# Optimization experiments

Measured on AMD Instinct MI355X. Metric: run time of the kernel, lower is better.

## Reference

```python
import jax, jax.numpy as jnp
import numpy as np

K = 16  # FLAGS.num_neighbors
N = 2562  # ellipsoid vertices
B = 4     # FLAGS.batch_size
M = 16384 # points per cloud
D = 3     # coordinate dim


def _mean_neighborhood(coord, pc, k):
    # coord: [N, D] query vertices; pc: [B, D, M] point cloud (channels-first)
    x2 = jnp.sum(coord * coord, axis=1)[None, :, None]          # [1, N, 1]
    y2 = jnp.sum(pc * pc, axis=1)[:, None, :]                   # [B, 1, M]
    xy = jnp.einsum('nd,bdm->bnm', coord, pc)                   # [B, N, M]
    d2 = x2 + y2 - 2.0 * xy                                     # [B, N, M]
    _, idx = jax.lax.top_k(-d2, k)                               # [B, N, K] indices into M
    Y = jnp.transpose(pc, (0, 2, 1))                             # [B, M, D]
    bv = jnp.arange(pc.shape[0])[:, None, None]                  # [B, 1, 1]
    knnY = Y[bv, idx]                                            # [B, N, K, D]
    knnY_mean = jnp.mean(knnY, axis=2)                           # [B, N, D]
    return knnY_mean[0]                                          # [N, D] (matches knnY_mean[0])


def setup_inputs() -> dict:
    key = jax.random.key(0)
    ks = jax.random.split(key, 5)
    inputs = jax.random.normal(ks[0], (N, D), dtype=jnp.float32)
    pcs = [jax.random.normal(ks[i + 1], (B, D, M), dtype=jnp.float32) for i in range(4)]
    return {"inputs": inputs, "pc0": pcs[0], "pc1": pcs[1], "pc2": pcs[2], "pc3": pcs[3]}


def reference(inputs, pc0, pc1, pc2, pc3):
    s0 = _mean_neighborhood(inputs, pc0, K)
    s1 = _mean_neighborhood(inputs, pc1, K)
    s2 = _mean_neighborhood(inputs, pc2, K)
    s3 = _mean_neighborhood(inputs, pc3, K)
    return jnp.concatenate([inputs, s0, s1, s2, s3], axis=1)  # [N, 5*D]
```

## Files before the change

kernel.cpp:

```cpp
#include <hip/hip_runtime.h>
#include <stdint.h>
#include <math.h>

#define NQ    2562
#define MPTS  16384
#define QPB   8
#define NBQ   321
#define NT    (MPTS / 256)
#define CAP   320

__global__ __launch_bounds__(256)
void passthrough_kernel(const float* __restrict__ inp, float* __restrict__ out) {
    int gid = blockIdx.x * 256 + threadIdx.x;
    if (gid < NQ * 3) {
        int n = gid / 3, c = gid - n * 3;
        out[n * 15 + c] = inp[gid];
    }
}

__device__ __forceinline__ float sqsum3(float y0, float y1, float y2) {
    return __fadd_rn(__fadd_rn(__fmul_rn(y0, y0), __fmul_rn(y1, y1)),
                     __fmul_rn(y2, y2));
}
__device__ __forceinline__ float keyf(float xs, float a2, float b2, float c2,
                                      float y0, float y1, float y2, float ysq) {
    float u = fmaf(c2, y2, fmaf(b2, y1, __fmul_rn(a2, y0)));
    return __fsub_rn(__fadd_rn(xs, ysq), u);
}
__device__ __forceinline__ unsigned long long packkey(float k, int m) {
    uint32_t kb = __float_as_uint(k);
    kb ^= (uint32_t)((int32_t)kb >> 31) | 0x80000000u;
    return ((unsigned long long)kb << 32) | (unsigned)m;
}
__device__ __forceinline__ float unmapkey(unsigned long long pk) {
    uint32_t kb = (uint32_t)(pk >> 32);
    return __uint_as_float((kb & 0x80000000u) ? (kb ^ 0x80000000u) : ~kb);
}
__device__ __forceinline__ int prefix_lt(unsigned long long m) {
    return __builtin_amdgcn_mbcnt_hi((unsigned)(m >> 32),
           __builtin_amdgcn_mbcnt_lo((unsigned)m, 0u));
}

__device__ __forceinline__ unsigned long long sort64(unsigned long long v, int lane) {
#pragma unroll
    for (int k = 2; k <= 64; k <<= 1) {
#pragma unroll
        for (int j = k >> 1; j > 0; j >>= 1) {
            unsigned long long p = __shfl_xor(v, j);
            bool up = ((lane & k) == 0) == ((lane & j) == 0);
            bool sw = up ? (p < v) : (v < p);
            v = sw ? p : v;
        }
    }
    return v;
}

__device__ __forceinline__ float rebuild_q(unsigned long long* t16p,
                                           unsigned* S, int& cnt, int lane,
                                           const float* __restrict__ P,
                                           float xs, float a2, float b2, float c2,
                                           bool fin) {
    int c = cnt;
    int full = c >> 6, rem = c & 63;
    int rounds = full + ((fin && rem) ? 1 : 0);
    unsigned long long v = ~0ULL;
    for (int rd = 0; rd < rounds; ++rd) {
        int i = (rd << 6) + lane;
        unsigned idx = (i < c) ? S[i] : 0u;
        float y0 = P[idx], y1 = P[MPTS + idx], y2 = P[2 * MPTS + idx];
        float key = keyf(xs, a2, b2, c2, y0, y1, y2, sqsum3(y0, y1, y2));
        unsigned long long pk = (i < c) ? packkey(key, (int)idx) : ~0ULL;
        pk = sort64(pk, lane);
        unsigned long long bsw = __shfl(pk, (31 - lane) & 63);
        v = (lane < 16) ? t16p[lane & 15] : (lane < 32) ? bsw : ~0ULL;
#pragma unroll
        for (int j = 16; j > 0; j >>= 1) {
            unsigned long long p2 = __shfl_xor(v, j);
            bool keepmin = (lane & j) == 0;
            bool less = p2 < v;
            v = (keepmin == less) ? p2 : v;
        }
        if (lane < 16) t16p[lane] = v;
    }
    if (!fin) {
        if (lane < rem) S[lane] = S[(full << 6) + lane];
        cnt = rem;
    } else {
        cnt = 0;
    }
    return unmapkey(__shfl(v, 15));
}

__global__ __launch_bounds__(256)
void knn_kernel(const float* __restrict__ inp,
                const float* __restrict__ pc0, const float* __restrict__ pc1,
                const float* __restrict__ pc2, const float* __restrict__ pc3,
                float* __restrict__ out) {
    const int b    = blockIdx.x;
    const int wid  = threadIdx.x >> 6;
    const int lane = threadIdx.x & 63;

    const int pc = b / NBQ;
    const int nb = b - pc * NBQ;
    const float* __restrict__ P = (pc == 0) ? pc0 : (pc == 1) ? pc1
                                : (pc == 2) ? pc2 : pc3;

    __shared__ unsigned           stk_sh[4][2][CAP];
    __shared__ unsigned long long t16_sh[4][2][16];

    if (lane < 32) t16_sh[wid][lane >> 4][lane & 15] = ~0ULL;

    float A2[2], B2[2], C2[2], XS[2];
#pragma unroll
    for (int r = 0; r < 2; ++r) {
        int n = QPB * nb + 2 * wid + r;
        n = (n < NQ) ? n : (NQ - 1);
        float x0 = inp[n * 3 + 0];
        float x1 = inp[n * 3 + 1];
        float x2 = inp[n * 3 + 2];
        A2[r] = 2.0f * x0;
        B2[r] = 2.0f * x1;
        C2[r] = 2.0f * x2;
        XS[r] = sqsum3(x0, x1, x2);
    }
    float tau[2];
    int   cnt[2] = {0, 0};

    const float* __restrict__ Pl = P + (lane << 2);

    auto push_tile = [&](int r, int mofs, float k0, float k1, float k2, float k3) {
        unsigned long long b0 = __ballot(k0 <= tau[r]);
        unsigned long long b1 = __ballot(k1 <= tau[r]);
        unsigned long long b2 = __ballot(k2 <= tau[r]);
        unsigned long long b3 = __ballot(k3 <= tau[r]);
        int pre = prefix_lt(b0) + prefix_lt(b1) + prefix_lt(b2) + prefix_lt(b3);
        int tot = __popcll(b0) + __popcll(b1) + __popcll(b2) + __popcll(b3);
        int pos = cnt[r] + pre;
        unsigned* S = stk_sh[wid][r];
        if (k0 <= tau[r]) S[pos++] = (unsigned)(mofs + 0);
        if (k1 <= tau[r]) S[pos++] = (unsigned)(mofs + 1);
        if (k2 <= tau[r]) S[pos++] = (unsigned)(mofs + 2);
        if (k3 <= tau[r]) S[pos++] = (unsigned)(mofs + 3);
        cnt[r] += tot;
        if (cnt[r] >= 64)
            tau[r] = rebuild_q(t16_sh[wid][r], S, cnt[r], lane,
                               P, XS[r], A2[r], B2[r], C2[r], false);
    };

    {
        float4 ax = *(const float4*)(Pl);
        float4 ay = *(const float4*)(Pl + MPTS);
        float4 az = *(const float4*)(Pl + 2 * MPTS);
        float q0 = sqsum3(ax.x, ay.x, az.x);
        float q1 = sqsum3(ax.y, ay.y, az.y);
        float q2 = sqsum3(ax.z, ay.z, az.z);
        float q3 = sqsum3(ax.w, ay.w, az.w);
#pragma unroll
        for (int r = 0; r < 2; ++r) {
            float k0 = keyf(XS[r], A2[r], B2[r], C2[r], ax.x, ay.x, az.x, q0);
            float k1 = keyf(XS[r], A2[r], B2[r], C2[r], ax.y, ay.y, az.y, q1);
            float k2 = keyf(XS[r], A2[r], B2[r], C2[r], ax.z, ay.z, az.z, q2);
            float k3 = keyf(XS[r], A2[r], B2[r], C2[r], ax.w, ay.w, az.w, q3);
            float km = fminf(fminf(k0, k1), fminf(k2, k3));
            float g = km;
            g = fminf(g, __shfl_xor(g, 1));
            g = fminf(g, __shfl_xor(g, 2));
            float m = g;
            m = fmaxf(m, __shfl_xor(m, 4));
            m = fmaxf(m, __shfl_xor(m, 8));
            m = fmaxf(m, __shfl_xor(m, 16));
            m = fmaxf(m, __shfl_xor(m, 32));
            tau[r] = m;
            push_tile(r, lane << 2, k0, k1, k2, k3);
        }
    }

    float4 cx = *(const float4*)(Pl + 256);
    float4 cy = *(const float4*)(Pl + MPTS + 256);
    float4 cz = *(const float4*)(Pl + 2 * MPTS + 256);

    for (int t = 1; t < NT; ++t) {
        const int tn = (t + 1 < NT) ? t + 1 : t;
        float4 nx = *(const float4*)(Pl + (tn << 8));
        float4 ny = *(const float4*)(Pl + MPTS + (tn << 8));
        float4 nz = *(const float4*)(Pl + 2 * MPTS + (tn << 8));

        const int mofs = (t << 8) + (lane << 2);
        float q0 = sqsum3(cx.x, cy.x, cz.x);
        float q1 = sqsum3(cx.y, cy.y, cz.y);
        float q2 = sqsum3(cx.z, cy.z, cz.z);
        float q3 = sqsum3(cx.w, cy.w, cz.w);
#pragma unroll
        for (int r = 0; r < 2; ++r) {
            float k0 = keyf(XS[r], A2[r], B2[r], C2[r], cx.x, cy.x, cz.x, q0);
            float k1 = keyf(XS[r], A2[r], B2[r], C2[r], cx.y, cy.y, cz.y, q1);
            float k2 = keyf(XS[r], A2[r], B2[r], C2[r], cx.z, cy.z, cz.z, q2);
            float k3 = keyf(XS[r], A2[r], B2[r], C2[r], cx.w, cy.w, cz.w, q3);
            float km = fminf(fminf(k0, k1), fminf(k2, k3));
            if (__ballot(km <= tau[r]))
                push_tile(r, mofs, k0, k1, k2, k3);
        }
        cx = nx; cy = ny; cz = nz;
    }

#pragma unroll
    for (int r = 0; r < 2; ++r) {
        if (cnt[r] > 0)
            rebuild_q(t16_sh[wid][r], stk_sh[wid][r], cnt[r], lane,
                      P, XS[r], A2[r], B2[r], C2[r], true);
    }

    {
        const int h   = lane >> 5;
        const int l32 = lane & 31;
        if (l32 < 16) {
            unsigned long long v = t16_sh[wid][h][l32];
            int idx = (int)(unsigned)v;
            float gx = P[idx];
            float gy = P[MPTS + idx];
            float gz = P[2 * MPTS + idx];
#pragma unroll
            for (int off = 8; off > 0; off >>= 1) {
                gx += __shfl_down(gx, off, 16);
                gy += __shfl_down(gy, off, 16);
                gz += __shfl_down(gz, off, 16);
            }
            if (l32 == 0) {
                int n = QPB * nb + 2 * wid + h;
                n = (n < NQ) ? n : (NQ - 1);
                float* o = out + n * 15 + 3 + 3 * pc;
                o[0] = gx * 0.0625f;
                o[1] = gy * 0.0625f;
                o[2] = gz * 0.0625f;
            }
        }
    }
}

extern "C" void kernel_launch(void* const* d_in, const int* in_sizes, int n_in,
                              void* d_out, int out_size, void* d_ws, size_t ws_size,
                              hipStream_t stream) {
    const float* inp = (const float*)d_in[0];
    const float* pc0 = (const float*)d_in[1];
    const float* pc1 = (const float*)d_in[2];
    const float* pc2 = (const float*)d_in[3];
    const float* pc3 = (const float*)d_in[4];
    float* out = (float*)d_out;

    hipLaunchKernelGGL(passthrough_kernel, dim3((NQ * 3 + 255) / 256), dim3(256),
                       0, stream, inp, out);

    hipLaunchKernelGGL(knn_kernel, dim3(4 * NBQ), dim3(256), 0, stream,
                       inp, pc0, pc1, pc2, pc3, out);
}
```

Before: 107.8 us.

## Process 512-point tiles per iteration and halve block size to 128 threads

Each warp now processes 8 candidate points per lane per iteration (two float4 groups 256 apart), so loop overhead and the ballot early-out check are amortized over twice as many points. Blocks shrink to 2 wavefronts (4 queries), doubling the block count, and the candidate stack capacity grows to hold up to 8 pushes per tile. The initial tau is now taken from the minimum over 8 points per lane, which makes it looser and can let more candidates through to rebuilds. Register pressure also rises from the extra prefetched float4s.

```diff
diff --git a/kernel.cpp b/kernel.cpp
--- a/kernel.cpp
+++ b/kernel.cpp
@@ -4,10 +4,10 @@
 
 #define NQ    2562
 #define MPTS  16384
-#define QPB   8
-#define NBQ   321
-#define NT    (MPTS / 256)
-#define CAP   320
+#define QPB   4
+#define NBQ   641
+#define NT    (MPTS / 512)
+#define CAP   576
 
 __global__ __launch_bounds__(256)
 void passthrough_kernel(const float* __restrict__ inp, float* __restrict__ out) {
@@ -91,7 +91,7 @@
     return unmapkey(__shfl(v, 15));
 }
 
-__global__ __launch_bounds__(256)
+__global__ __launch_bounds__(128)
 void knn_kernel(const float* __restrict__ inp,
                 const float* __restrict__ pc0, const float* __restrict__ pc1,
                 const float* __restrict__ pc2, const float* __restrict__ pc3,
@@ -105,8 +105,8 @@
     const float* __restrict__ P = (pc == 0) ? pc0 : (pc == 1) ? pc1
                                 : (pc == 2) ? pc2 : pc3;
 
-    __shared__ unsigned           stk_sh[4][2][CAP];
-    __shared__ unsigned long long t16_sh[4][2][16];
+    __shared__ unsigned           stk_sh[2][2][CAP];
+    __shared__ unsigned long long t16_sh[2][2][16];
 
     if (lane < 32) t16_sh[wid][lane >> 4][lane & 15] = ~0ULL;
 
@@ -128,79 +128,82 @@
 
     const float* __restrict__ Pl = P + (lane << 2);
 
-    auto push_tile = [&](int r, int mofs, float k0, float k1, float k2, float k3) {
-        unsigned long long b0 = __ballot(k0 <= tau[r]);
-        unsigned long long b1 = __ballot(k1 <= tau[r]);
-        unsigned long long b2 = __ballot(k2 <= tau[r]);
-        unsigned long long b3 = __ballot(k3 <= tau[r]);
-        int pre = prefix_lt(b0) + prefix_lt(b1) + prefix_lt(b2) + prefix_lt(b3);
-        int tot = __popcll(b0) + __popcll(b1) + __popcll(b2) + __popcll(b3);
+    auto push8 = [&](int r, int base0, const float* k) {
+        unsigned long long bm[8];
+        int pre = 0, tot = 0;
+#pragma unroll
+        for (int i = 0; i < 8; ++i) {
+            bm[i] = __ballot(k[i] <= tau[r]);
+            pre += prefix_lt(bm[i]);
+            tot += __popcll(bm[i]);
+        }
         int pos = cnt[r] + pre;
         unsigned* S = stk_sh[wid][r];
-        if (k0 <= tau[r]) S[pos++] = (unsigned)(mofs + 0);
-        if (k1 <= tau[r]) S[pos++] = (unsigned)(mofs + 1);
-        if (k2 <= tau[r]) S[pos++] = (unsigned)(mofs + 2);
-        if (k3 <= tau[r]) S[pos++] = (unsigned)(mofs + 3);
+#pragma unroll
+        for (int i = 0; i < 8; ++i)
+            if (k[i] <= tau[r]) S[pos++] = (unsigned)(base0 + (i < 4 ? i : i + 252));
         cnt[r] += tot;
         if (cnt[r] >= 64)
             tau[r] = rebuild_q(t16_sh[wid][r], S, cnt[r], lane,
                                P, XS[r], A2[r], B2[r], C2[r], false);
     };
 
-    {
-        float4 ax = *(const float4*)(Pl);
-        float4 ay = *(const float4*)(Pl + MPTS);
-        float4 az = *(const float4*)(Pl + 2 * MPTS);
-        float q0 = sqsum3(ax.x, ay.x, az.x);
-        float q1 = sqsum3(ax.y, ay.y, az.y);
-        float q2 = sqsum3(ax.z, ay.z, az.z);
-        float q3 = sqsum3(ax.w, ay.w, az.w);
+    float4 cx0, cx1, cy0, cy1, cz0, cz1;
+    cx0 = *(const float4*)(Pl);             cx1 = *(const float4*)(Pl + 256);
+    cy0 = *(const float4*)(Pl + MPTS);      cy1 = *(const float4*)(Pl + MPTS + 256);
+    cz0 = *(const float4*)(Pl + 2*MPTS);    cz1 = *(const float4*)(Pl + 2*MPTS + 256);
+
+    for (int t = 0; t < NT; ++t) {
+        const int tn = (t + 1 < NT) ? t + 1 : t;
+        const int po = tn << 9;
+        float4 nx0 = *(const float4*)(Pl + po);
+        float4 nx1 = *(const float4*)(Pl + po + 256);
+        float4 ny0 = *(const float4*)(Pl + MPTS + po);
+        float4 ny1 = *(const float4*)(Pl + MPTS + po + 256);
+        float4 nz0 = *(const float4*)(Pl + 2*MPTS + po);
+        float4 nz1 = *(const float4*)(Pl + 2*MPTS + po + 256);
+
+        const int base0 = (t << 9) + (lane << 2);
+        float q[8];
+        q[0] = sqsum3(cx0.x, cy0.x, cz0.x);
+        q[1] = sqsum3(cx0.y, cy0.y, cz0.y);
+        q[2] = sqsum3(cx0.z, cy0.z, cz0.z);
+        q[3] = sqsum3(cx0.w, cy0.w, cz0.w);
+        q[4] = sqsum3(cx1.x, cy1.x, cz1.x);
+        q[5] = sqsum3(cx1.y, cy1.y, cz1.y);
+        q[6] = sqsum3(cx1.z, cy1.z, cz1.z);
+        q[7] = sqsum3(cx1.w, cy1.w, cz1.w);
+
 #pragma unroll
         for (int r = 0; r < 2; ++r) {
-            float k0 = keyf(XS[r], A2[r], B2[r], C2[r], ax.x, ay.x, az.x, q0);
-            float k1 = keyf(XS[r], A2[r], B2[r], C2[r], ax.y, ay.y, az.y, q1);
-            float k2 = keyf(XS[r], A2[r], B2[r], C2[r], ax.z, ay.z, az.z, q2);
-            float k3 = keyf(XS[r], A2[r], B2[r], C2[r], ax.w, ay.w, az.w, q3);
-            float km = fminf(fminf(k0, k1), fminf(k2, k3));
-            float g = km;
-            g = fminf(g, __shfl_xor(g, 1));
-            g = fminf(g, __shfl_xor(g, 2));
-            float m = g;
-            m = fmaxf(m, __shfl_xor(m, 4));
-            m = fmaxf(m, __shfl_xor(m, 8));
-            m = fmaxf(m, __shfl_xor(m, 16));
-            m = fmaxf(m, __shfl_xor(m, 32));
-            tau[r] = m;
-            push_tile(r, lane << 2, k0, k1, k2, k3);
-        }
-    }
-
-    float4 cx = *(const float4*)(Pl + 256);
-    float4 cy = *(const float4*)(Pl + MPTS + 256);
-    float4 cz = *(const float4*)(Pl + 2 * MPTS + 256);
-
-    for (int t = 1; t < NT; ++t) {
-        const int tn = (t + 1 < NT) ? t + 1 : t;
-        float4 nx = *(const float4*)(Pl + (tn << 8));
-        float4 ny = *(const float4*)(Pl + MPTS + (tn << 8));
-        float4 nz = *(const float4*)(Pl + 2 * MPTS + (tn << 8));
-
-        const int mofs = (t << 8) + (lane << 2);
-        float q0 = sqsum3(cx.x, cy.x, cz.x);
-        float q1 = sqsum3(cx.y, cy.y, cz.y);
-        float q2 = sqsum3(cx.z, cy.z, cz.z);
-        float q3 = sqsum3(cx.w, cy.w, cz.w);
-#pragma unroll
-        for (int r = 0; r < 2; ++r) {
-            float k0 = keyf(XS[r], A2[r], B2[r], C2[r], cx.x, cy.x, cz.x, q0);
-            float k1 = keyf(XS[r], A2[r], B2[r], C2[r], cx.y, cy.y, cz.y, q1);
-            float k2 = keyf(XS[r], A2[r], B2[r], C2[r], cx.z, cy.z, cz.z, q2);
-            float k3 = keyf(XS[r], A2[r], B2[r], C2[r], cx.w, cy.w, cz.w, q3);
-            float km = fminf(fminf(k0, k1), fminf(k2, k3));
-            if (__ballot(km <= tau[r]))
-                push_tile(r, mofs, k0, k1, k2, k3);
-        }
-        cx = nx; cy = ny; cz = nz;
+            float k[8];
+            k[0] = keyf(XS[r], A2[r], B2[r], C2[r], cx0.x, cy0.x, cz0.x, q[0]);
+            k[1] = keyf(XS[r], A2[r], B2[r], C2[r], cx0.y, cy0.y, cz0.y, q[1]);
+            k[2] = keyf(XS[r], A2[r], B2[r], C2[r], cx0.z, cy0.z, cz0.z, q[2]);
+            k[3] = keyf(XS[r], A2[r], B2[r], C2[r], cx0.w, cy0.w, cz0.w, q[3]);
+            k[4] = keyf(XS[r], A2[r], B2[r], C2[r], cx1.x, cy1.x, cz1.x, q[4]);
+            k[5] = keyf(XS[r], A2[r], B2[r], C2[r], cx1.y, cy1.y, cz1.y, q[5]);
+            k[6] = keyf(XS[r], A2[r], B2[r], C2[r], cx1.z, cy1.z, cz1.z, q[6]);
+            k[7] = keyf(XS[r], A2[r], B2[r], C2[r], cx1.w, cy1.w, cz1.w, q[7]);
+            float km = fminf(fminf(fminf(k[0], k[1]), fminf(k[2], k[3])),
+                             fminf(fminf(k[4], k[5]), fminf(k[6], k[7])));
+
+            if (t == 0) {
+                float g = km;
+                g = fminf(g, __shfl_xor(g, 1));
+                g = fminf(g, __shfl_xor(g, 2));
+                float m = g;
+                m = fmaxf(m, __shfl_xor(m, 4));
+                m = fmaxf(m, __shfl_xor(m, 8));
+                m = fmaxf(m, __shfl_xor(m, 16));
+                m = fmaxf(m, __shfl_xor(m, 32));
+                tau[r] = m;
+                push8(r, base0, k);
+            } else if (__ballot(km <= tau[r])) {
+                push8(r, base0, k);
+            }
+        }
+        cx0 = nx0; cx1 = nx1; cy0 = ny0; cy1 = ny1; cz0 = nz0; cz1 = nz1;
     }
 
 #pragma unroll
@@ -250,6 +253,6 @@
     hipLaunchKernelGGL(passthrough_kernel, dim3((NQ * 3 + 255) / 256), dim3(256),
                        0, stream, inp, out);
 
-    hipLaunchKernelGGL(knn_kernel, dim3(4 * NBQ), dim3(256), 0, stream,
+    hipLaunchKernelGGL(knn_kernel, dim3(4 * NBQ), dim3(128), 0, stream,
                        inp, pc0, pc1, pc2, pc3, out);
 }
```

New measurement: 120.9 us. +12.2%, slower.
